# Optimization experiments

Hardware: AMD Instinct MI355X
Metric: run time of the kernel (lower is better)

## Reference

```python
import jax, jax.numpy as jnp
import numpy as np

B = 1024       # graphs per batch
N = 64         # nodes (fields) per graph
D_IN = 64      # field embedding dim
HID = 128      # hidden_dim
HEADS = 4      # num_heads
E_RAND = 448   # random template edges per graph (plus N self loops)
LN_EPS = 1e-5
NEG_SLOPE = 0.2


def setup_inputs() -> dict:
    key = jax.random.key(0)
    ks = jax.random.split(key, 16)
    rng = np.random.default_rng(0)

    # --- batched edge_index: same template graph replicated with node offsets ---
    src_t = rng.integers(0, N, E_RAND)
    dst_t = rng.integers(0, N, E_RAND)
    loops = np.arange(N)
    src_t = np.concatenate([src_t, loops])   # self loops (PyG GATConv default)
    dst_t = np.concatenate([dst_t, loops])
    offs = (np.arange(B) * N)[:, None]
    src = (src_t[None, :] + offs).reshape(-1)
    dst = (dst_t[None, :] + offs).reshape(-1)
    edge_index = jnp.asarray(np.stack([src, dst]), dtype=jnp.int32)  # [2, E]
    batch_idx = jnp.repeat(jnp.arange(B, dtype=jnp.int32), N)        # [B*N]

    s = 0.05
    inp = {
        "field_vecs": jax.random.normal(ks[0], (B, N, D_IN), jnp.float32),
        "W_align": jax.random.normal(ks[1], (D_IN, HID), jnp.float32) * s,
        "b_align": jnp.zeros((HID,), jnp.float32),
        "ln_gamma": jnp.ones((HID,), jnp.float32),
        "ln_beta": jnp.zeros((HID,), jnp.float32),
        "mask_logits": jnp.full((N,), 2.2, jnp.float32),
        "W1": jax.random.normal(ks[2], (HID, HEADS * HID), jnp.float32) * s,
        "att_src1": jax.random.normal(ks[3], (HEADS, HID), jnp.float32) * s,
        "att_dst1": jax.random.normal(ks[4], (HEADS, HID), jnp.float32) * s,
        "bias1": jnp.zeros((HEADS * HID,), jnp.float32),
        "W2": jax.random.normal(ks[5], (HEADS * HID, HID), jnp.float32) * s,
        "att_src2": jax.random.normal(ks[6], (1, HID), jnp.float32) * s,
        "att_dst2": jax.random.normal(ks[7], (1, HID), jnp.float32) * s,
        "bias2": jnp.zeros((HID,), jnp.float32),
        "edge_index": edge_index,
        "batch_idx": batch_idx,
    }
    return inp


def gat_conv(x, edge_index, W, att_src, att_dst, bias, heads, out_dim, concat):
    num_nodes = x.shape[0]
    h = (x @ W).reshape(num_nodes, heads, out_dim)          # [V,H,D]
    src, dst = edge_index[0], edge_index[1]
    a_src = jnp.einsum('vhd,hd->vh', h, att_src)            # [V,H]
    a_dst = jnp.einsum('vhd,hd->vh', h, att_dst)
    e = jax.nn.leaky_relu(a_src[src] + a_dst[dst], NEG_SLOPE)  # [E,H]
    # segment softmax over incoming edges of each dst node
    emax = jax.ops.segment_max(e, dst, num_segments=num_nodes)
    e = jnp.exp(e - emax[dst])
    denom = jax.ops.segment_sum(e, dst, num_segments=num_nodes)
    alpha = e / (denom[dst] + 1e-16)                        # [E,H]
    msg = h[src] * alpha[:, :, None]                        # [E,H,D]
    out = jax.ops.segment_sum(msg, dst, num_segments=num_nodes)
    if concat:
        out = out.reshape(num_nodes, heads * out_dim)
    else:
        out = out.mean(axis=1)
    return out + bias


def reference(field_vecs, W_align, b_align, ln_gamma, ln_beta, mask_logits,
              W1, att_src1, att_dst1, bias1, W2, att_src2, att_dst2, bias2,
              edge_index, batch_idx):
    # align fields: Linear(d_in -> hidden) on [B,N,d_in]
    x = jnp.einsum('bnd,dh->bnh', field_vecs, W_align) + b_align
    # LayerNorm over hidden
    mu = x.mean(-1, keepdims=True)
    var = ((x - mu) ** 2).mean(-1, keepdims=True)
    x = (x - mu) * jax.lax.rsqrt(var + LN_EPS) * ln_gamma + ln_beta
    # per-node learnable feature gate
    feature_gate = jax.nn.sigmoid(mask_logits)              # [N]
    x = x * feature_gate[None, :, None]
    x = x.reshape(-1, HID)                                  # [B*N, HID]
    # GAT layer 1 (concat heads) + ELU, GAT layer 2 (mean heads)
    x = gat_conv(x, edge_index, W1, att_src1, att_dst1, bias1, HEADS, HID, True)
    x = jax.nn.elu(x)
    x = gat_conv(x, edge_index, W2, att_src2, att_dst2, bias2, 1, HID, False)
    # global mean pool per graph
    counts = jax.ops.segment_sum(jnp.ones_like(batch_idx, jnp.float32), batch_idx, num_segments=B)
    graph_embedding = jax.ops.segment_sum(x, batch_idx, num_segments=B) / counts[:, None]
    return graph_embedding, feature_gate
```

## Files before the change

kernel.cpp:

```cpp
#include <hip/hip_runtime.h>
#include <math.h>

#define B_ 1024
#define N_ 64
#define DIN 64
#define HID 128
#define HEADS 4
#define EPG 512
#define ETOT (B_ * EPG)
#define LN_EPS 1e-5f
#define NEG_SLOPE 0.2f
#define NT 512

typedef _Float16 f16;
typedef _Float16 f16x8 __attribute__((ext_vector_type(8)));
typedef _Float16 f16x4 __attribute__((ext_vector_type(4)));
typedef float f32x4 __attribute__((ext_vector_type(4)));

__device__ int g_off[65];
__device__ int g_srcs[EPG];

__device__ __forceinline__ float wave_sum(float v) {
#pragma unroll
    for (int o = 32; o > 0; o >>= 1) v += __shfl_xor(v, o);
    return v;
}

#define SWZ(row, byteoff) ((byteoff) ^ (((row) & 7) << 4))

#define OFF_XF16   0
#define OFF_BUFA   16384
#define OFF_X1     49152
#define OFF_ALPHA  114688
#define OFF_SRCS   116736
#define OFF_OFFS   117760
#define OFF_SASRC  118032
#define OFF_SADST  118288
#define OFF_SDEN   118544
#define LDS_BYTES  118800

__global__ void k_prep(const int* __restrict__ edge_index) {
    __shared__ unsigned cnt[64], cur[64];
    __shared__ int soff[65];
    const int t = threadIdx.x;
    if (t < 64) cnt[t] = 0u;
    __syncthreads();
    const int sv = edge_index[t];
    const int dv = edge_index[ETOT + t];
    atomicAdd(&cnt[dv], 1u);
    __syncthreads();
    if (t == 0) {
        int a = 0;
        for (int v = 0; v < 64; ++v) { soff[v] = a; cur[v] = (unsigned)a; a += (int)cnt[v]; }
        soff[64] = a;
    }
    __syncthreads();
    const unsigned p = atomicAdd(&cur[dv], 1u);
    g_srcs[p] = sv;
    if (t < 65) g_off[t] = soff[t];
}

__global__ __launch_bounds__(512) void k_prepw(
    const float* __restrict__ W1, const float* __restrict__ W2,
    f16* __restrict__ W1T, f16* __restrict__ W2T)
{
    const int tid = blockIdx.x * 512 + threadIdx.x;
    if (tid < 65536) {
        const int h = tid >> 14, n = (tid >> 7) & 127, k = tid & 127;
        W1T[tid] = (f16)W1[(size_t)k * 512 + h * 128 + n];
    } else {
        const int i = tid - 65536;
        const int n = i >> 9, k = i & 511;
        W2T[i] = (f16)W2[(size_t)k * 128 + n];
    }
}

__device__ __forceinline__ void stage_wt(unsigned char* smem,
                                         const unsigned char* src, int srcRowBytes, int t)
{
#pragma unroll
    for (int j = 0; j < 4; ++j) {
        const int gi = t + j * 512;
        const int row = gi >> 4, c16 = gi & 15;
        *(float4*)(smem + OFF_BUFA + row * 256 + SWZ(row, c16 * 16)) =
            *(const float4*)(src + (size_t)row * srcRowBytes + c16 * 16);
    }
}

__device__ __forceinline__ void mma_tiles(const unsigned char* smem, int abase, int arow,
                                          int kstep0, int ksteps, int t, f32x4 acc[4])
{
    const int lane = t & 63, w = t >> 6;
    const int arownum = (w & 3) * 16 + (lane & 15);
    const int brow0 = (w >> 2) * 64 + (lane & 15);
    const int kb = (lane >> 4) * 16;
    for (int ks = kstep0; ks < kstep0 + ksteps; ++ks) {
        const f16x8 a = *(const f16x8*)(smem + abase + (size_t)arownum * arow +
                                        SWZ(arownum, ks * 64 + kb));
#pragma unroll
        for (int i = 0; i < 4; ++i) {
            const int br = brow0 + i * 16;
            const f16x8 b = *(const f16x8*)(smem + OFF_BUFA + br * 256 +
                                            SWZ(br, (ks - kstep0) * 64 + kb));
            acc[i] = __builtin_amdgcn_mfma_f32_16x16x32_f16(a, b, acc[i], 0, 0, 0);
        }
    }
}

__device__ __forceinline__ void write_c(unsigned char* smem, int t, const f32x4 acc[4])
{
    const int lane = t & 63, w = t >> 6;
    float* hb = (float*)(smem + OFF_BUFA);
    const int r0 = (w & 3) * 16 + (lane >> 4) * 4;
#pragma unroll
    for (int i = 0; i < 4; ++i) {
        const int col = (w >> 2) * 64 + i * 16 + (lane & 15);
#pragma unroll
        for (int r = 0; r < 4; ++r) hb[(size_t)(r0 + r) * HID + col] = acc[i][r];
    }
}

__global__ __launch_bounds__(NT, 1) void k_fused(
    const float* __restrict__ fv, const float* __restrict__ Wal,
    const float* __restrict__ bal, const float* __restrict__ gam,
    const float* __restrict__ bet, const float* __restrict__ ml,
    const f16* __restrict__ W1T, const float* __restrict__ as1,
    const float* __restrict__ ad1, const float* __restrict__ b1,
    const f16* __restrict__ W2T, const float* __restrict__ as2,
    const float* __restrict__ ad2, const float* __restrict__ b2,
    float* __restrict__ out)
{
    __shared__ __align__(16) unsigned char smem[LDS_BYTES];
    const int t = threadIdx.x, lane = t & 63, w = t >> 6;
    const int g = blockIdx.x;

    float* bufaF = (float*)(smem + OFF_BUFA);
    float* fvs   = (float*)(smem + OFF_X1);
    float* alpha = (float*)(smem + OFF_ALPHA);
    short* srcs  = (short*)(smem + OFF_SRCS);
    int*   offs  = (int*)(smem + OFF_OFFS);
    float* sasrc = (float*)(smem + OFF_SASRC);
    float* sadst = (float*)(smem + OFF_SADST);
    float* sden  = (float*)(smem + OFF_SDEN);

    srcs[t] = (short)g_srcs[t];
    if (t < 65) offs[t] = g_off[t];
    {
        const float4* s4 = (const float4*)(fv + (size_t)g * 64 * DIN);
        float4* d4 = (float4*)fvs;
        d4[t] = s4[t]; d4[t + 512] = s4[t + 512];
        const float4* w4 = (const float4*)Wal;
        float4* b4 = (float4*)bufaF;
#pragma unroll
        for (int j = 0; j < 4; ++j) b4[t + j * 512] = w4[t + j * 512];
    }
    __syncthreads();

    {
        const float blo = bal[lane], bhi = bal[64 + lane];
        const float glo = gam[lane], ghi = gam[64 + lane];
        const float belo = bet[lane], behi = bet[64 + lane];
        for (int n = w * 8; n < w * 8 + 8; ++n) {
            float a0 = 0.f, a1 = 0.f;
#pragma unroll 8
            for (int k = 0; k < DIN; ++k) {
                const float f = fvs[n * DIN + k];
                a0 += f * bufaF[k * HID + lane];
                a1 += f * bufaF[k * HID + 64 + lane];
            }
            a0 += blo; a1 += bhi;
            const float mu = wave_sum(a0 + a1) * (1.f / HID);
            const float c0 = a0 - mu, c1 = a1 - mu;
            const float var = wave_sum(c0 * c0 + c1 * c1) * (1.f / HID);
            const float rs = rsqrtf(var + LN_EPS);
            const float gt = 1.f / (1.f + expf(-ml[n]));
            *(f16*)(smem + OFF_XF16 + n * 256 + SWZ(n, lane * 2)) = (f16)((c0 * rs * glo + belo) * gt);
            *(f16*)(smem + OFF_XF16 + n * 256 + SWZ(n, 128 + lane * 2)) = (f16)((c1 * rs * ghi + behi) * gt);
        }
    }
    if (g == 0 && t < 64) out[(size_t)B_ * HID + t] = 1.f / (1.f + expf(-ml[t]));
    __syncthreads();

    for (int h = 0; h < HEADS; ++h) {
        stage_wt(smem, (const unsigned char*)(W1T + (size_t)h * 128 * 128), 256, t);
        __syncthreads();
        f32x4 acc[4];
#pragma unroll
        for (int i = 0; i < 4; ++i) acc[i] = (f32x4){0.f, 0.f, 0.f, 0.f};
        mma_tiles(smem, OFF_XF16, 256, 0, 4, t, acc);
        __syncthreads();
        write_c(smem, t, acc);
        __syncthreads();

        {
            const float s0 = as1[h * HID + lane], s1v = as1[h * HID + 64 + lane];
            const float d0 = ad1[h * HID + lane], d1v = ad1[h * HID + 64 + lane];
            for (int i = w * 8; i < w * 8 + 8; ++i) {
                const float h0 = bufaF[i * HID + lane], h1v = bufaF[i * HID + 64 + lane];
                const float vs = wave_sum(h0 * s0 + h1v * s1v);
                const float vd = wave_sum(h0 * d0 + h1v * d1v);
                if (lane == 0) { sasrc[i] = vs; sadst[i] = vd; }
            }
        }
        __syncthreads();

        {
            const int g8 = t >> 3, sl = t & 7;
            const int b = offs[g8], e = offs[g8 + 1];
            const float sad = sadst[g8];
            float mx = -1e30f;
            for (int i = b + sl; i < e; i += 8) {
                float sc = sasrc[srcs[i]] + sad;
                sc = sc > 0.f ? sc : NEG_SLOPE * sc;
                alpha[i] = sc;
                mx = fmaxf(mx, sc);
            }
#pragma unroll
            for (int o = 1; o < 8; o <<= 1) mx = fmaxf(mx, __shfl_xor(mx, o));
            float den = 0.f;
            for (int i = b + sl; i < e; i += 8) {
                const float ex = expf(alpha[i] - mx);
                alpha[i] = ex;
                den += ex;
            }
#pragma unroll
            for (int o = 1; o < 8; o <<= 1) den += __shfl_xor(den, o);
            if (sl == 0) sden[g8] = 1.f / (den + 1e-16f);
        }
        __syncthreads();

        {
            const int grp = t >> 5, l32 = t & 31, c = l32 * 4;
            const float4 bv = *(const float4*)&b1[h * HID + c];
            for (int d = grp; d < 64; d += 16) {
                const int b = offs[d], e = offs[d + 1];
                const float rd = sden[d];
                float a0 = 0.f, a1 = 0.f, a2 = 0.f, a3 = 0.f;
                for (int i = b; i < e; ++i) {
                    const float al = alpha[i];
                    const float4 hv = *(const float4*)&bufaF[(size_t)srcs[i] * HID + c];
                    a0 += al * hv.x; a1 += al * hv.y; a2 += al * hv.z; a3 += al * hv.w;
                }
                float o0 = a0 * rd + bv.x, o1 = a1 * rd + bv.y;
                float o2 = a2 * rd + bv.z, o3 = a3 * rd + bv.w;
                o0 = o0 > 0.f ? o0 : expm1f(o0);
                o1 = o1 > 0.f ? o1 : expm1f(o1);
                o2 = o2 > 0.f ? o2 : expm1f(o2);
                o3 = o3 > 0.f ? o3 : expm1f(o3);
                f16x4 p; p.x = (f16)o0; p.y = (f16)o1; p.z = (f16)o2; p.w = (f16)o3;
                *(f16x4*)(smem + OFF_X1 + d * 1024 + SWZ(d, h * 256 + c * 2)) = p;
            }
        }
        __syncthreads();
    }

    f32x4 acc2[4];
#pragma unroll
    for (int i = 0; i < 4; ++i) acc2[i] = (f32x4){0.f, 0.f, 0.f, 0.f};
    for (int kc = 0; kc < 4; ++kc) {
        stage_wt(smem, (const unsigned char*)W2T + (size_t)kc * 256, 1024, t);
        __syncthreads();
        mma_tiles(smem, OFF_X1, 1024, kc * 4, 4, t, acc2);
        __syncthreads();
    }
    write_c(smem, t, acc2);
    __syncthreads();

    {
        const float s0 = as2[lane], s1v = as2[64 + lane];
        const float d0 = ad2[lane], d1v = ad2[64 + lane];
        for (int i = w * 8; i < w * 8 + 8; ++i) {
            const float h0 = bufaF[i * HID + lane], h1v = bufaF[i * HID + 64 + lane];
            const float vs = wave_sum(h0 * s0 + h1v * s1v);
            const float vd = wave_sum(h0 * d0 + h1v * d1v);
            if (lane == 0) { sasrc[i] = vs; sadst[i] = vd; }
        }
    }
    __syncthreads();
    {
        const int g8 = t >> 3, sl = t & 7;
        const int b = offs[g8], e = offs[g8 + 1];
        const float sad = sadst[g8];
        float mx = -1e30f;
        for (int i = b + sl; i < e; i += 8) {
            float sc = sasrc[srcs[i]] + sad;
            sc = sc > 0.f ? sc : NEG_SLOPE * sc;
            alpha[i] = sc;
            mx = fmaxf(mx, sc);
        }
#pragma unroll
        for (int o = 1; o < 8; o <<= 1) mx = fmaxf(mx, __shfl_xor(mx, o));
        float den = 0.f;
        for (int i = b + sl; i < e; i += 8) {
            const float ex = expf(alpha[i] - mx);
            alpha[i] = ex;
            den += ex;
        }
#pragma unroll
        for (int o = 1; o < 8; o <<= 1) den += __shfl_xor(den, o);
        if (sl == 0) sden[g8] = 1.f / (den + 1e-16f);
    }
    __syncthreads();

    {
        const int grp = t >> 5, l32 = t & 31, c = l32 * 4;
        float p0 = 0.f, p1 = 0.f, p2 = 0.f, p3 = 0.f;
        for (int d = grp; d < 64; d += 16) {
            const int b = offs[d], e = offs[d + 1];
            const float rd = sden[d];
            float a0 = 0.f, a1 = 0.f, a2 = 0.f, a3 = 0.f;
            for (int i = b; i < e; ++i) {
                const float al = alpha[i];
                const float4 hv = *(const float4*)&bufaF[(size_t)srcs[i] * HID + c];
                a0 += al * hv.x; a1 += al * hv.y; a2 += al * hv.z; a3 += al * hv.w;
            }
            p0 += a0 * rd; p1 += a1 * rd; p2 += a2 * rd; p3 += a3 * rd;
        }
        float* pool = (float*)(smem + OFF_X1);
        *(float4*)&pool[(size_t)grp * HID + c] = make_float4(p0, p1, p2, p3);
    }
    __syncthreads();
    if (t < HID) {
        const float* pool = (const float*)(smem + OFF_X1);
        float s = 0.f;
#pragma unroll
        for (int i = 0; i < 16; ++i) s += pool[(size_t)i * HID + t];
        out[(size_t)g * HID + t] = s * (1.f / 64.f) + b2[t];
    }
}

extern "C" void kernel_launch(void* const* d_in, const int* in_sizes, int n_in,
                              void* d_out, int out_size, void* d_ws, size_t ws_size,
                              hipStream_t stream)
{
    (void)in_sizes; (void)n_in; (void)out_size; (void)ws_size;
    const float* fv        = (const float*)d_in[0];
    const float* W_align   = (const float*)d_in[1];
    const float* b_align   = (const float*)d_in[2];
    const float* ln_gamma  = (const float*)d_in[3];
    const float* ln_beta   = (const float*)d_in[4];
    const float* mask_log  = (const float*)d_in[5];
    const float* W1        = (const float*)d_in[6];
    const float* att_src1  = (const float*)d_in[7];
    const float* att_dst1  = (const float*)d_in[8];
    const float* bias1     = (const float*)d_in[9];
    const float* W2        = (const float*)d_in[10];
    const float* att_src2  = (const float*)d_in[11];
    const float* att_dst2  = (const float*)d_in[12];
    const float* bias2     = (const float*)d_in[13];
    const int*   edge_idx  = (const int*)d_in[14];

    float* out = (float*)d_out;
    f16* W1T = (f16*)d_ws;
    f16* W2T = W1T + 65536;

    k_prep<<<1, EPG, 0, stream>>>(edge_idx);
    k_prepw<<<256, 512, 0, stream>>>(W1, W2, W1T, W2T);
    k_fused<<<B_, NT, 0, stream>>>(fv, W_align, b_align, ln_gamma, ln_beta, mask_log,
                                   W1T, att_src1, att_dst1, bias1,
                                   W2T, att_src2, att_dst2, bias2, out);
}
```

Measured before the change: 348.7 us.

## Stream MFMA weights from global, interleave layer-2 GEMM per head, cut LDS for 2 blocks/CU

The MFMA B operands (W1T, W2T) are now read directly from global/L2 instead of being staged through LDS, and the layer-2 GEMM is accumulated per head right after that head's aggregation. The full 64x512 fp16 layer-1 output buffer therefore shrinks to a 64x128 slice. LDS drops from about 116KB to about 68KB, and launch bounds now request 2 blocks per CU for more occupancy and fewer barriers. The align GEMM is register-blocked over 8 nodes, and expf becomes __expf. The trade-off is uncached, uncoalesced global weight reads inside the MFMA loop, plus slightly lower exp precision.

```diff
diff --git a/kernel.cpp b/kernel.cpp
--- a/kernel.cpp
+++ b/kernel.cpp
@@ -29,15 +29,15 @@
 #define SWZ(row, byteoff) ((byteoff) ^ (((row) & 7) << 4))
 
 #define OFF_XF16   0
-#define OFF_BUFA   16384
-#define OFF_X1     49152
-#define OFF_ALPHA  114688
-#define OFF_SRCS   116736
-#define OFF_OFFS   117760
-#define OFF_SASRC  118032
-#define OFF_SADST  118288
-#define OFF_SDEN   118544
-#define LDS_BYTES  118800
+#define OFF_H32    16384
+#define OFF_X1H    49152
+#define OFF_ALPHA  65536
+#define OFF_SRCS   67584
+#define OFF_OFFS   68608
+#define OFF_SASRC  68880
+#define OFF_SADST  69136
+#define OFF_SDEN   69392
+#define LDS_BYTES  69648
 
 __global__ void k_prep(const int* __restrict__ edge_index) {
     __shared__ unsigned cnt[64], cur[64];
@@ -75,33 +75,20 @@
     }
 }
 
-__device__ __forceinline__ void stage_wt(unsigned char* smem,
-                                         const unsigned char* src, int srcRowBytes, int t)
-{
-#pragma unroll
-    for (int j = 0; j < 4; ++j) {
-        const int gi = t + j * 512;
-        const int row = gi >> 4, c16 = gi & 15;
-        *(float4*)(smem + OFF_BUFA + row * 256 + SWZ(row, c16 * 16)) =
-            *(const float4*)(src + (size_t)row * srcRowBytes + c16 * 16);
-    }
-}
-
-__device__ __forceinline__ void mma_tiles(const unsigned char* smem, int abase, int arow,
-                                          int kstep0, int ksteps, int t, f32x4 acc[4])
+__device__ __forceinline__ void mma_g(const unsigned char* smem, int abase,
+                                      const f16* __restrict__ B, int bstride,
+                                      int t, f32x4 acc[4])
 {
     const int lane = t & 63, w = t >> 6;
-    const int arownum = (w & 3) * 16 + (lane & 15);
-    const int brow0 = (w >> 2) * 64 + (lane & 15);
-    const int kb = (lane >> 4) * 16;
-    for (int ks = kstep0; ks < kstep0 + ksteps; ++ks) {
-        const f16x8 a = *(const f16x8*)(smem + abase + (size_t)arownum * arow +
-                                        SWZ(arownum, ks * 64 + kb));
+    const int am = (w & 3) * 16 + (lane & 15);
+    const int bn = (w >> 2) * 64 + (lane & 15);
+    const int ke = (lane >> 4) * 8;
+#pragma unroll
+    for (int ks = 0; ks < 4; ++ks) {
+        const f16x8 a = *(const f16x8*)(smem + abase + am * 256 + SWZ(am, ks * 64 + ke * 2));
 #pragma unroll
         for (int i = 0; i < 4; ++i) {
-            const int br = brow0 + i * 16;
-            const f16x8 b = *(const f16x8*)(smem + OFF_BUFA + br * 256 +
-                                            SWZ(br, (ks - kstep0) * 64 + kb));
+            const f16x8 b = *(const f16x8*)(B + (size_t)(bn + i * 16) * bstride + ks * 32 + ke);
             acc[i] = __builtin_amdgcn_mfma_f32_16x16x32_f16(a, b, acc[i], 0, 0, 0);
         }
     }
@@ -110,7 +97,7 @@
 __device__ __forceinline__ void write_c(unsigned char* smem, int t, const f32x4 acc[4])
 {
     const int lane = t & 63, w = t >> 6;
-    float* hb = (float*)(smem + OFF_BUFA);
+    float* hb = (float*)(smem + OFF_H32);
     const int r0 = (w & 3) * 16 + (lane >> 4) * 4;
 #pragma unroll
     for (int i = 0; i < 4; ++i) {
@@ -120,7 +107,7 @@
     }
 }
 
-__global__ __launch_bounds__(NT, 1) void k_fused(
+__global__ __launch_bounds__(NT, 2) void k_fused(
     const float* __restrict__ fv, const float* __restrict__ Wal,
     const float* __restrict__ bal, const float* __restrict__ gam,
     const float* __restrict__ bet, const float* __restrict__ ml,
@@ -134,8 +121,7 @@
     const int t = threadIdx.x, lane = t & 63, w = t >> 6;
     const int g = blockIdx.x;
 
-    float* bufaF = (float*)(smem + OFF_BUFA);
-    float* fvs   = (float*)(smem + OFF_X1);
+    float* hF    = (float*)(smem + OFF_H32);
     float* alpha = (float*)(smem + OFF_ALPHA);
     short* srcs  = (short*)(smem + OFF_SRCS);
     int*   offs  = (int*)(smem + OFF_OFFS);
@@ -147,48 +133,64 @@
     if (t < 65) offs[t] = g_off[t];
     {
         const float4* s4 = (const float4*)(fv + (size_t)g * 64 * DIN);
-        float4* d4 = (float4*)fvs;
+        float4* d4 = (float4*)(smem + OFF_X1H);
         d4[t] = s4[t]; d4[t + 512] = s4[t + 512];
         const float4* w4 = (const float4*)Wal;
-        float4* b4 = (float4*)bufaF;
+        float4* b4 = (float4*)hF;
 #pragma unroll
         for (int j = 0; j < 4; ++j) b4[t + j * 512] = w4[t + j * 512];
     }
     __syncthreads();
 
     {
-        const float blo = bal[lane], bhi = bal[64 + lane];
-        const float glo = gam[lane], ghi = gam[64 + lane];
+        const float* fvs = (const float*)(smem + OFF_X1H);
+        const int nb = w * 8;
+        float acc0[8], acc1[8];
+#pragma unroll
+        for (int n = 0; n < 8; ++n) { acc0[n] = 0.f; acc1[n] = 0.f; }
+        for (int k4 = 0; k4 < 16; ++k4) {
+            const int k = k4 * 4;
+            const float wl0 = hF[(k + 0) * HID + lane], wh0 = hF[(k + 0) * HID + 64 + lane];
+            const float wl1 = hF[(k + 1) * HID + lane], wh1 = hF[(k + 1) * HID + 64 + lane];
+            const float wl2 = hF[(k + 2) * HID + lane], wh2 = hF[(k + 2) * HID + 64 + lane];
+            const float wl3 = hF[(k + 3) * HID + lane], wh3 = hF[(k + 3) * HID + 64 + lane];
+#pragma unroll
+            for (int n = 0; n < 8; ++n) {
+                const float4 f = *(const float4*)&fvs[(nb + n) * DIN + k];
+                acc0[n] += f.x * wl0 + f.y * wl1 + f.z * wl2 + f.w * wl3;
+                acc1[n] += f.x * wh0 + f.y * wh1 + f.z * wh2 + f.w * wh3;
+            }
+        }
+        const float blo = bal[lane],  bhi = bal[64 + lane];
+        const float glo = gam[lane],  ghi = gam[64 + lane];
         const float belo = bet[lane], behi = bet[64 + lane];
-        for (int n = w * 8; n < w * 8 + 8; ++n) {
-            float a0 = 0.f, a1 = 0.f;
-#pragma unroll 8
-            for (int k = 0; k < DIN; ++k) {
-                const float f = fvs[n * DIN + k];
-                a0 += f * bufaF[k * HID + lane];
-                a1 += f * bufaF[k * HID + 64 + lane];
-            }
-            a0 += blo; a1 += bhi;
+#pragma unroll
+        for (int n = 0; n < 8; ++n) {
+            const int node = nb + n;
+            const float a0 = acc0[n] + blo, a1 = acc1[n] + bhi;
             const float mu = wave_sum(a0 + a1) * (1.f / HID);
             const float c0 = a0 - mu, c1 = a1 - mu;
             const float var = wave_sum(c0 * c0 + c1 * c1) * (1.f / HID);
             const float rs = rsqrtf(var + LN_EPS);
-            const float gt = 1.f / (1.f + expf(-ml[n]));
-            *(f16*)(smem + OFF_XF16 + n * 256 + SWZ(n, lane * 2)) = (f16)((c0 * rs * glo + belo) * gt);
-            *(f16*)(smem + OFF_XF16 + n * 256 + SWZ(n, 128 + lane * 2)) = (f16)((c1 * rs * ghi + behi) * gt);
-        }
-    }
-    if (g == 0 && t < 64) out[(size_t)B_ * HID + t] = 1.f / (1.f + expf(-ml[t]));
-    __syncthreads();
+            const float gt = 1.f / (1.f + __expf(-ml[node]));
+            *(f16*)(smem + OFF_XF16 + node * 256 + SWZ(node, lane * 2)) =
+                (f16)((c0 * rs * glo + belo) * gt);
+            *(f16*)(smem + OFF_XF16 + node * 256 + SWZ(node, 128 + lane * 2)) =
+                (f16)((c1 * rs * ghi + behi) * gt);
+        }
+    }
+    if (g == 0 && t < 64) out[(size_t)B_ * HID + t] = 1.f / (1.f + __expf(-ml[t]));
+    __syncthreads();
+
+    f32x4 acc2[4];
+#pragma unroll
+    for (int i = 0; i < 4; ++i) acc2[i] = (f32x4){0.f, 0.f, 0.f, 0.f};
 
     for (int h = 0; h < HEADS; ++h) {
-        stage_wt(smem, (const unsigned char*)(W1T + (size_t)h * 128 * 128), 256, t);
-        __syncthreads();
         f32x4 acc[4];
 #pragma unroll
         for (int i = 0; i < 4; ++i) acc[i] = (f32x4){0.f, 0.f, 0.f, 0.f};
-        mma_tiles(smem, OFF_XF16, 256, 0, 4, t, acc);
-        __syncthreads();
+        mma_g(smem, OFF_XF16, W1T + (size_t)h * HID * HID, HID, t, acc);
         write_c(smem, t, acc);
         __syncthreads();
 
@@ -196,7 +198,7 @@
             const float s0 = as1[h * HID + lane], s1v = as1[h * HID + 64 + lane];
             const float d0 = ad1[h * HID + lane], d1v = ad1[h * HID + 64 + lane];
             for (int i = w * 8; i < w * 8 + 8; ++i) {
-                const float h0 = bufaF[i * HID + lane], h1v = bufaF[i * HID + 64 + lane];
+                const float h0 = hF[i * HID + lane], h1v = hF[i * HID + 64 + lane];
                 const float vs = wave_sum(h0 * s0 + h1v * s1v);
                 const float vd = wave_sum(h0 * d0 + h1v * d1v);
                 if (lane == 0) { sasrc[i] = vs; sadst[i] = vd; }
@@ -219,7 +221,7 @@
             for (int o = 1; o < 8; o <<= 1) mx = fmaxf(mx, __shfl_xor(mx, o));
             float den = 0.f;
             for (int i = b + sl; i < e; i += 8) {
-                const float ex = expf(alpha[i] - mx);
+                const float ex = __expf(alpha[i] - mx);
                 alpha[i] = ex;
                 den += ex;
             }
@@ -238,7 +240,7 @@
                 float a0 = 0.f, a1 = 0.f, a2 = 0.f, a3 = 0.f;
                 for (int i = b; i < e; ++i) {
                     const float al = alpha[i];
-                    const float4 hv = *(const float4*)&bufaF[(size_t)srcs[i] * HID + c];
+                    const float4 hv = *(const float4*)&hF[(size_t)srcs[i] * HID + c];
                     a0 += al * hv.x; a1 += al * hv.y; a2 += al * hv.z; a3 += al * hv.w;
                 }
                 float o0 = a0 * rd + bv.x, o1 = a1 * rd + bv.y;
@@ -248,29 +250,21 @@
                 o2 = o2 > 0.f ? o2 : expm1f(o2);
                 o3 = o3 > 0.f ? o3 : expm1f(o3);
                 f16x4 p; p.x = (f16)o0; p.y = (f16)o1; p.z = (f16)o2; p.w = (f16)o3;
-                *(f16x4*)(smem + OFF_X1 + d * 1024 + SWZ(d, h * 256 + c * 2)) = p;
+                *(f16x4*)(smem + OFF_X1H + d * 256 + SWZ(d, c * 2)) = p;
             }
         }
         __syncthreads();
-    }
-
-    f32x4 acc2[4];
-#pragma unroll
-    for (int i = 0; i < 4; ++i) acc2[i] = (f32x4){0.f, 0.f, 0.f, 0.f};
-    for (int kc = 0; kc < 4; ++kc) {
-        stage_wt(smem, (const unsigned char*)W2T + (size_t)kc * 256, 1024, t);
-        __syncthreads();
-        mma_tiles(smem, OFF_X1, 1024, kc * 4, 4, t, acc2);
-        __syncthreads();
-    }
+
+        mma_g(smem, OFF_X1H, W2T + (size_t)h * HID, 4 * HID, t, acc2);
+    }
+
     write_c(smem, t, acc2);
     __syncthreads();
-
     {
         const float s0 = as2[lane], s1v = as2[64 + lane];
         const float d0 = ad2[lane], d1v = ad2[64 + lane];
         for (int i = w * 8; i < w * 8 + 8; ++i) {
-            const float h0 = bufaF[i * HID + lane], h1v = bufaF[i * HID + 64 + lane];
+            const float h0 = hF[i * HID + lane], h1v = hF[i * HID + 64 + lane];
             const float vs = wave_sum(h0 * s0 + h1v * s1v);
             const float vd = wave_sum(h0 * d0 + h1v * d1v);
             if (lane == 0) { sasrc[i] = vs; sadst[i] = vd; }
@@ -292,7 +286,7 @@
         for (int o = 1; o < 8; o <<= 1) mx = fmaxf(mx, __shfl_xor(mx, o));
         float den = 0.f;
         for (int i = b + sl; i < e; i += 8) {
-            const float ex = expf(alpha[i] - mx);
+            const float ex = __expf(alpha[i] - mx);
             alpha[i] = ex;
             den += ex;
         }
@@ -311,17 +305,17 @@
             float a0 = 0.f, a1 = 0.f, a2 = 0.f, a3 = 0.f;
             for (int i = b; i < e; ++i) {
                 const float al = alpha[i];
-                const float4 hv = *(const float4*)&bufaF[(size_t)srcs[i] * HID + c];
+                const float4 hv = *(const float4*)&hF[(size_t)srcs[i] * HID + c];
                 a0 += al * hv.x; a1 += al * hv.y; a2 += al * hv.z; a3 += al * hv.w;
             }
             p0 += a0 * rd; p1 += a1 * rd; p2 += a2 * rd; p3 += a3 * rd;
         }
-        float* pool = (float*)(smem + OFF_X1);
+        float* pool = (float*)(smem + OFF_X1H);
         *(float4*)&pool[(size_t)grp * HID + c] = make_float4(p0, p1, p2, p3);
     }
     __syncthreads();
     if (t < HID) {
-        const float* pool = (const float*)(smem + OFF_X1);
+        const float* pool = (const float*)(smem + OFF_X1H);
         float s = 0.f;
 #pragma unroll
         for (int i = 0; i < 16; ++i) s += pool[(size_t)i * HID + t];
```

After: 302.7 us. -13.2%, faster.
